# Kernel optimization log

Measured on AMD Instinct MI355X. Metric: run time of the kernel, lower is better.

## Reference

```python
import jax, jax.numpy as jnp
import numpy as np

L, B, D, H, K = 1024, 64, 256, 256, 4  # nodes, batch, input dim, hidden dim, heap arity


def _build_tree_schedule():
    # Deterministic 4-ary heap tree: parent(i) = (i-1)//K; children 4i+1..4i+4.
    # First K//2 children are 'left', last K//2 are 'right'. Pad slots use index L
    # (a sentinel zero row). Levels are processed deepest-first (leaves -> root).
    depth = np.zeros(L, dtype=np.int64)
    for i in range(1, L):
        depth[i] = depth[(i - 1) // K] + 1
    n_levels = int(depth.max()) + 1
    levels = [np.where(depth == d)[0] for d in range(n_levels)]
    M = max(len(lv) for lv in levels)
    level_nodes = np.full((n_levels, M), L, dtype=np.int32)
    child_idx = np.full((n_levels, M, K), L, dtype=np.int32)
    for d, lv in enumerate(levels):
        level_nodes[d, : len(lv)] = lv
        for j, n in enumerate(lv):
            for c in range(K):
                cc = K * n + c + 1
                if cc < L:
                    child_idx[d, j, c] = cc
    return jnp.asarray(level_nodes), jnp.asarray(child_idx)


def setup_inputs() -> dict:
    key = jax.random.key(0)
    ks = jax.random.split(key, 9)
    level_nodes, child_idx = _build_tree_schedule()
    sD = 1.0 / np.sqrt(D).astype(np.float32)
    sH = 1.0 / np.sqrt(H).astype(np.float32)
    return {
        "inputs": jax.random.normal(ks[0], (L, B, D), jnp.float32),
        "level_nodes": level_nodes,
        "child_idx": child_idx,
        "W_gih": jax.random.normal(ks[1], (5 * H, D), jnp.float32) * sD,
        "b_gih": jax.random.normal(ks[2], (5 * H,), jnp.float32) * sD,
        "W_glh": jax.random.normal(ks[3], (5 * H, H), jnp.float32) * sH,
        "W_grh": jax.random.normal(ks[4], (5 * H, H), jnp.float32) * sH,
        "W_cih": jax.random.normal(ks[5], (H, D), jnp.float32) * sD,
        "b_cih": jax.random.normal(ks[6], (H,), jnp.float32) * sD,
        "W_clh": jax.random.normal(ks[7], (H, H), jnp.float32) * sH,
        "W_crh": jax.random.normal(ks[8], (H, H), jnp.float32) * sH,
    }


def _tree_gru(inputs, level_nodes, child_idx, W_gih, b_gih, W_glh, W_grh,
              W_cih, b_cih, W_clh, W_crh):
    Ln, Bn, Dn = inputs.shape
    Hn = W_cih.shape[0]
    # Sentinel zero row at index Ln for padded node/child slots.
    inp_p = jnp.concatenate([inputs, jnp.zeros((1, Bn, Dn), inputs.dtype)], axis=0)
    h = jnp.zeros((Bn, Ln + 1, Hn), inputs.dtype)
    n_levels = level_nodes.shape[0]
    half = K // 2
    for d in range(n_levels - 1, -1, -1):  # leaves first, root last
        nodes = level_nodes[d]             # [M]
        ch = child_idx[d]                  # [M, K]
        # gather + sum child hidden states per side
        left_h = h[:, ch[:, 0]] + h[:, ch[:, 1]]      # [B, M, H]
        right_h = h[:, ch[:, half]] + h[:, ch[:, half + 1]]
        x = jnp.transpose(inp_p[nodes], (1, 0, 2))    # [B, M, D]
        gates = jax.nn.sigmoid(x @ W_gih.T + b_gih + left_h @ W_glh.T + right_h @ W_grh.T)
        rl, rr, zl, zr, z = jnp.split(gates, 5, axis=-1)
        cell = jnp.tanh(x @ W_cih.T + b_cih + (rl * left_h) @ W_clh.T + (rr * right_h) @ W_crh.T)
        hidden = zl * left_h + zr * right_h + z * cell
        h = h.at[:, nodes].set(hidden)
        h = h.at[:, Ln].set(0.0)  # keep sentinel row zero (padded writes land here)
    hn = h[:, :Ln]  # [B, L, H]
    # original output order: nodes 1..L-1 then root (node 0)
    outputs = jnp.concatenate([hn[:, 1:], hn[:, :1]], axis=1)
    return outputs, hn[:, 0]


def reference(inputs, level_nodes, child_idx, W_gih, b_gih, W_glh, W_grh,
              W_cih, b_cih, W_clh, W_crh):
    return _tree_gru(inputs, level_nodes, child_idx, W_gih, b_gih, W_glh, W_grh,
                     W_cih, b_cih, W_clh, W_crh)
```

## Files before the change

kernel.cpp:

```cpp
#include <hip/hip_runtime.h>


#define L_TOT 1024

typedef __attribute__((ext_vector_type(8))) short short8;
typedef __attribute__((ext_vector_type(4))) short short4v;
typedef __attribute__((ext_vector_type(4))) float f32x4;

static __device__ __forceinline__ float bf2f(unsigned short u) {
  unsigned int x = ((unsigned int)u) << 16;
  return __builtin_bit_cast(float, x);
}
static __device__ __forceinline__ unsigned short f2bf(float f) {
  unsigned int u = __builtin_bit_cast(unsigned int, f);
  u += 0x7fffu + ((u >> 16) & 1u);
  return (unsigned short)(u >> 16);
}
static __device__ __forceinline__ float sigmf(float x) { return 1.0f / (1.0f + __expf(-x)); }
static __device__ __forceinline__ float tanhf_(float x) { return 2.0f / (1.0f + __expf(-2.0f * x)) - 1.0f; }

static __device__ __forceinline__ void bar_lgkm() {
  asm volatile("s_waitcnt lgkmcnt(0)" ::: "memory");
  __builtin_amdgcn_s_barrier();
  __builtin_amdgcn_sched_barrier(0);
}

static __device__ __forceinline__ int swz_t(int orig, int nwg) {
  int q = nwg >> 3, r = nwg & 7, x = orig & 7, s = orig >> 3;
  return (x < r ? x * (q + 1) : r * (q + 1) + (x - r) * q) + s;
}

__global__ __launch_bounds__(256) void k_pre(
    const float* __restrict__ in,
    const float* __restrict__ Wgih, const float* __restrict__ Wglh, const float* __restrict__ Wgrh,
    const float* __restrict__ Wcih, const float* __restrict__ Wclh, const float* __restrict__ Wcrh,
    unsigned short* __restrict__ xb, unsigned short* __restrict__ Wg,
    unsigned short* __restrict__ Wc, unsigned short* __restrict__ Wl,
    unsigned short* __restrict__ hb) {
  int t = blockIdx.x * 256 + threadIdx.x;
  if (t < 524288) {
    const float* s = in + (size_t)t * 8;
    short8 v;
#pragma unroll
    for (int j = 0; j < 8; ++j) v[j] = (short)f2bf(s[j]);
    *(short8*)(xb + (size_t)t * 8) = v;
  }
  const int NG = 1280 * 768;
  const int NC = 256 * 768;
  const int NL = 512 * 256;
  if (t < NG) {
    int g = t / 768, k = t % 768;
    float v = (k < 256) ? Wgih[g * 256 + k] : ((k < 512) ? Wglh[g * 256 + k - 256] : Wgrh[g * 256 + k - 512]);
    Wg[t] = f2bf(v);
  } else if (t < NG + NC) {
    int t2 = t - NG;
    int g = t2 / 768, k = t2 % 768;
    float v = (k < 256) ? Wcih[g * 256 + k] : ((k < 512) ? Wclh[g * 256 + k - 256] : Wcrh[g * 256 + k - 512]);
    Wc[t2] = f2bf(v);
  } else if (t < NG + NC + NL) {
    int t2 = t - NG - NC;
    int n = t2 >> 8, k = t2 & 255;
    int g = n >> 4;
    int hc = (g >> 1) * 16 + (n & 15);
    float v = (g & 1) ? Wcih[hc * 256 + k] : Wgih[(1024 + hc) * 256 + k];
    Wl[t2] = f2bf(v);
  }
  if (t < 16384) hb[(size_t)1024 * 16384 + t] = 0;
}

__global__ __launch_bounds__(256) void k_prep(const unsigned short* __restrict__ hb,
                                              unsigned short* __restrict__ lh,
                                              unsigned short* __restrict__ rh,
                                              int rows, int row_off, int lvl_start) {
  int t = blockIdx.x * 256 + threadIdx.x;
  if (t >= rows * 32) return;
  int r = t >> 5, k8 = (t & 31) << 3;
  int gr = row_off + r;
  int node = lvl_start + (gr >> 6);
  int b = gr & 63;
  int cb = 4 * node + 1;
  int c0 = cb, c1 = cb + 1, c2 = cb + 2, c3 = cb + 3;
  c0 = (c0 < L_TOT) ? c0 : L_TOT;
  c1 = (c1 < L_TOT) ? c1 : L_TOT;
  c2 = (c2 < L_TOT) ? c2 : L_TOT;
  c3 = (c3 < L_TOT) ? c3 : L_TOT;
  const short8 v0 = *(const short8*)(hb + (size_t)c0 * 16384 + b * 256 + k8);
  const short8 v1 = *(const short8*)(hb + (size_t)c1 * 16384 + b * 256 + k8);
  const short8 v2 = *(const short8*)(hb + (size_t)c2 * 16384 + b * 256 + k8);
  const short8 v3 = *(const short8*)(hb + (size_t)c3 * 16384 + b * 256 + k8);
  short8 ol, orr;
#pragma unroll
  for (int j = 0; j < 8; ++j) {
    ol[j] = (short)f2bf(bf2f((unsigned short)v0[j]) + bf2f((unsigned short)v1[j]));
    orr[j] = (short)f2bf(bf2f((unsigned short)v2[j]) + bf2f((unsigned short)v3[j]));
  }
  *(short8*)(lh + (size_t)r * 256 + k8) = ol;
  *(short8*)(rh + (size_t)r * 256 + k8) = orr;
}

template <int EPI>
static __device__ __forceinline__ void gemm_body(
    const float* __restrict__ Af,
    const unsigned short* __restrict__ Aseg0,
    const unsigned short* __restrict__ Aseg1,
    const unsigned short* __restrict__ Aseg2,
    const unsigned short* __restrict__ Wt, const float* __restrict__ bias,
    const float* __restrict__ bias2,
    int rows, int row_off, int lvl_start, int NT, int nwg,
    const unsigned short* __restrict__ lh, const unsigned short* __restrict__ rh,
    unsigned short* __restrict__ a2l, unsigned short* __restrict__ a2r,
    unsigned short* __restrict__ p1, unsigned short* __restrict__ p2,
    unsigned short* __restrict__ zb, unsigned short* __restrict__ hb,
    float* __restrict__ out) {
  constexpr int NKT = (EPI == 2) ? 4 : 12;
  constexpr int WSTRIDE = (EPI == 2) ? 256 : 768;
  constexpr int LR = 72;
  int t = swz_t(blockIdx.x, nwg);
  int tm = t / NT, tn = t % NT;
  const int tid = threadIdx.x, lane = tid & 63, wave = tid >> 6;
  const int wr = wave >> 1, wcl = wave & 1;

  __shared__ unsigned short As[2][128 * LR];
  __shared__ unsigned short Bs[2][128 * LR];

  f32x4 acc[2][4];
#pragma unroll
  for (int i = 0; i < 2; ++i)
#pragma unroll
    for (int j = 0; j < 4; ++j) {
      f32x4 zv = {0.f, 0.f, 0.f, 0.f};
      acc[i][j] = zv;
    }

  const unsigned short* segs[3] = {Aseg0, Aseg1, Aseg2};
  const int srow = tid >> 3;
  const int scol = (tid & 7) * 8;

  short8 rva[3][2], rvb[3][2];
  f32x4 fva[3][2][2];

  auto LOADK = [&](int kt, int s) {
    int ko = (kt & 3) * 64;
#pragma unroll
    for (int i = 0; i < 2; ++i) {
      int row = srow + i * 64;
      if (EPI == 2) {
        const float* ap = Af + (size_t)(tm * 128 + row) * 256 + ko + scol;
        fva[s][i][0] = *(const f32x4*)(ap);
        fva[s][i][1] = *(const f32x4*)(ap + 4);
      } else {
        const unsigned short* segp = segs[kt >> 2];
        rva[s][i] = *(const short8*)(segp + (size_t)(tm * 128 + row) * 256 + ko + scol);
      }
      rvb[s][i] = *(const short8*)(Wt + (size_t)(tn * 128 + row) * WSTRIDE + kt * 64 + scol);
    }
  };
  auto WRITEK = [&](int s, int buf) {
#pragma unroll
    for (int i = 0; i < 2; ++i) {
      int row = srow + i * 64;
      short8 v;
      if (EPI == 2) {
#pragma unroll
        for (int j = 0; j < 4; ++j) {
          v[j] = (short)f2bf(fva[s][i][0][j]);
          v[j + 4] = (short)f2bf(fva[s][i][1][j]);
        }
      } else {
        v = rva[s][i];
      }
      *(short8*)(&As[buf][row * LR + scol]) = v;
      *(short8*)(&Bs[buf][row * LR + scol]) = rvb[s][i];
    }
  };

  LOADK(0, 0);
  LOADK(1, 1);
  if (NKT > 2) LOADK(2, 2);
  WRITEK(0, 0);
  bar_lgkm();

#pragma unroll
  for (int kt = 0; kt < NKT; ++kt) {
    const int cur = kt & 1;
    if (kt + 1 < NKT) WRITEK((kt + 1) % 3, cur ^ 1);
    if (kt + 3 < NKT) LOADK(kt + 3, kt % 3);
#pragma unroll
    for (int kk = 0; kk < 2; ++kk) {
      short8 af[2], bf[4];
#pragma unroll
      for (int mf = 0; mf < 2; ++mf)
        af[mf] = *(const short8*)(&As[cur][(wr * 32 + mf * 16 + (lane & 15)) * LR + kk * 32 + (lane >> 4) * 8]);
#pragma unroll
      for (int nf = 0; nf < 4; ++nf)
        bf[nf] = *(const short8*)(&Bs[cur][(wcl * 64 + nf * 16 + (lane & 15)) * LR + kk * 32 + (lane >> 4) * 8]);
#pragma unroll
      for (int mf = 0; mf < 2; ++mf)
#pragma unroll
        for (int nf = 0; nf < 4; ++nf)
          acc[mf][nf] = __builtin_amdgcn_mfma_f32_16x16x32_bf16(bf[nf], af[mf], acc[mf][nf], 0, 0, 0);
    }
    if (kt + 1 < NKT) bar_lgkm();
  }

  if (EPI == 2) {
#pragma unroll
    for (int nfp = 0; nfp < 2; ++nfp) {
      int nz = nfp * 2;
      int g = tn * 8 + wcl * 4 + nz;
      int hcq = (g >> 1) * 16 + (lane >> 4) * 4;
      f32x4 bzv = *(const f32x4*)(bias + 1024 + hcq);
      f32x4 bcv = *(const f32x4*)(bias2 + hcq);
#pragma unroll
      for (int mf = 0; mf < 2; ++mf) {
        int r = tm * 128 + wr * 32 + mf * 16 + (lane & 15);
        int node = 256 + (r >> 6), b = r & 63;
        short4v hv;
        float4 ov;
#pragma unroll
        for (int j = 0; j < 4; ++j) {
          float h = sigmf(acc[mf][nz][j] + bzv[j]) * tanhf_(acc[mf][nz + 1][j] + bcv[j]);
          hv[j] = (short)f2bf(h);
          ((float*)&ov)[j] = h;
        }
        *(short4v*)(hb + (size_t)node * 16384 + b * 256 + hcq) = hv;
        *(float4*)(out + (size_t)b * 262144 + (size_t)(node - 1) * 256 + hcq) = ov;
      }
    }
    return;
  }
#pragma unroll
  for (int nf = 0; nf < 4; ++nf) {
    int colq = tn * 128 + wcl * 64 + nf * 16 + (lane >> 4) * 4;
    f32x4 bsv = *(const f32x4*)(bias + colq);
    if (EPI == 0) {
      int ck = colq >> 8;
      int gcq = colq & 255;
#pragma unroll
      for (int mf = 0; mf < 2; ++mf) {
        int r = tm * 128 + wr * 32 + mf * 16 + (lane & 15);
        if (r < rows) {
          size_t idx = (size_t)r * 256 + gcq;
          f32x4 s;
#pragma unroll
          for (int j = 0; j < 4; ++j) s[j] = sigmf(acc[mf][nf][j] + bsv[j]);
          short4v res;
          if (ck == 4) {
#pragma unroll
            for (int j = 0; j < 4; ++j) res[j] = (short)f2bf(s[j]);
            *(short4v*)(zb + idx) = res;
          } else {
            const unsigned short* src = (ck == 0 || ck == 2) ? lh : rh;
            short4v hv = *(const short4v*)(src + idx);
#pragma unroll
            for (int j = 0; j < 4; ++j) res[j] = (short)f2bf(s[j] * bf2f((unsigned short)hv[j]));
            if (ck == 0)      *(short4v*)(a2l + idx) = res;
            else if (ck == 1) *(short4v*)(a2r + idx) = res;
            else if (ck == 2) *(short4v*)(p1 + idx) = res;
            else              *(short4v*)(p2 + idx) = res;
          }
        }
      }
    } else {
#pragma unroll
      for (int mf = 0; mf < 2; ++mf) {
        int r = tm * 128 + wr * 32 + mf * 16 + (lane & 15);
        if (r < rows) {
          size_t idx = (size_t)r * 256 + colq;
          short4v p1v = *(const short4v*)(p1 + idx);
          short4v p2v = *(const short4v*)(p2 + idx);
          short4v zbv = *(const short4v*)(zb + idx);
          int gr = row_off + r;
          int node = lvl_start + (gr >> 6);
          int b = gr & 63;
          short4v hv;
          float4 ov;
#pragma unroll
          for (int j = 0; j < 4; ++j) {
            float cell = tanhf_(acc[mf][nf][j] + bsv[j]);
            float hid = bf2f((unsigned short)p1v[j]) + bf2f((unsigned short)p2v[j]) +
                        bf2f((unsigned short)zbv[j]) * cell;
            hv[j] = (short)f2bf(hid);
            ((float*)&ov)[j] = hid;
          }
          *(short4v*)(hb + (size_t)node * 16384 + b * 256 + colq) = hv;
          int jj = node ? (node - 1) : 1023;
          *(float4*)(out + (size_t)b * 262144 + (size_t)jj * 256 + colq) = ov;
          if (node == 0)
            *(float4*)(out + 16777216 + (size_t)b * 256 + colq) = ov;
        }
      }
    }
  }
}

__global__ __launch_bounds__(512, 4) void k_gates(
    const unsigned short* __restrict__ A0, const unsigned short* __restrict__ A1,
    const unsigned short* __restrict__ A2, const unsigned short* __restrict__ Wt,
    const float* __restrict__ bias, int rows, int row_off, int lvl_start, int nwg,
    const unsigned short* __restrict__ lh, const unsigned short* __restrict__ rh,
    unsigned short* __restrict__ a2l, unsigned short* __restrict__ a2r,
    unsigned short* __restrict__ p1, unsigned short* __restrict__ p2,
    unsigned short* __restrict__ zb) {
  gemm_body<0>(nullptr, A0, A1, A2, Wt, bias, nullptr, rows, row_off, lvl_start, 10, nwg,
               lh, rh, a2l, a2r, p1, p2, zb, nullptr, nullptr);
}

__global__ __launch_bounds__(512, 4) void k_cell(
    const unsigned short* __restrict__ A0, const unsigned short* __restrict__ A1,
    const unsigned short* __restrict__ A2, const unsigned short* __restrict__ Wt,
    const float* __restrict__ bias, int rows, int row_off, int lvl_start, int nwg,
    const unsigned short* __restrict__ p1, const unsigned short* __restrict__ p2,
    const unsigned short* __restrict__ zb, unsigned short* __restrict__ hb,
    float* __restrict__ out) {
  gemm_body<1>(nullptr, A0, A1, A2, Wt, bias, nullptr, rows, row_off, lvl_start, 2, nwg,
               nullptr, nullptr, nullptr, nullptr, (unsigned short*)p1,
               (unsigned short*)p2, (unsigned short*)zb, hb, out);
}

__global__ __launch_bounds__(512, 4) void k_leaf(
    const float* __restrict__ X, const unsigned short* __restrict__ Wl,
    const float* __restrict__ bg, const float* __restrict__ bc, int nwg,
    unsigned short* __restrict__ hb, float* __restrict__ out) {
  gemm_body<2>(X, nullptr, nullptr, nullptr, Wl, bg, bc, 49152, 0, 0, 4, nwg,
               nullptr, nullptr, nullptr, nullptr, nullptr, nullptr, nullptr, hb, out);
}

extern "C" void kernel_launch(void* const* d_in, const int* in_sizes, int n_in,
                              void* d_out, int out_size, void* d_ws, size_t ws_size,
                              hipStream_t stream) {
  const float* inputs = (const float*)d_in[0];
  const float* W_gih = (const float*)d_in[3];
  const float* b_gih = (const float*)d_in[4];
  const float* W_glh = (const float*)d_in[5];
  const float* W_grh = (const float*)d_in[6];
  const float* W_cih = (const float*)d_in[7];
  const float* b_cih = (const float*)d_in[8];
  const float* W_clh = (const float*)d_in[9];
  const float* W_crh = (const float*)d_in[10];
  float* out = (float*)d_out;

  char* ws = (char*)d_ws;
  size_t cur = 0;
  auto alloc = [&](size_t bytes) -> char* {
    char* p = ws + cur;
    cur += (bytes + 255) & ~(size_t)255;
    return p;
  };

  unsigned short* xb = (unsigned short*)alloc((size_t)(16384 + 128) * 256 * 2);
  unsigned short* hb = (unsigned short*)alloc((size_t)1025 * 16384 * 2);
  unsigned short* Wg = (unsigned short*)alloc((size_t)1280 * 768 * 2);
  unsigned short* Wc = (unsigned short*)alloc((size_t)256 * 768 * 2);
  unsigned short* Wl = (unsigned short*)alloc((size_t)512 * 256 * 2);

  size_t rem = (ws_size > cur) ? (ws_size - cur) : 0;
  long long rcap = (long long)(rem / (7 * 512 + 64));
  rcap = (rcap / 128) * 128;
  int Rchunk = (int)((rcap < 11008) ? rcap : 11008);
  if (Rchunk < 128) Rchunk = 128;

  unsigned short* lh  = (unsigned short*)alloc((size_t)Rchunk * 512);
  unsigned short* rh  = (unsigned short*)alloc((size_t)Rchunk * 512);
  unsigned short* a2l = (unsigned short*)alloc((size_t)Rchunk * 512);
  unsigned short* a2r = (unsigned short*)alloc((size_t)Rchunk * 512);
  unsigned short* p1  = (unsigned short*)alloc((size_t)Rchunk * 512);
  unsigned short* p2  = (unsigned short*)alloc((size_t)Rchunk * 512);
  unsigned short* zb  = (unsigned short*)alloc((size_t)Rchunk * 512);

  k_pre<<<5120, 256, 0, stream>>>(inputs, W_gih, W_glh, W_grh, W_cih, W_clh, W_crh,
                                  xb, Wg, Wc, Wl, hb);

  k_leaf<<<1536, 512, 0, stream>>>(inputs + (size_t)16384 * 256, Wl, b_gih, b_cih, 1536, hb, out);

  static const int LSi[5] = {0, 1, 5, 21, 85};
  static const int LCi[5] = {1, 4, 16, 64, 171};

  for (int d = 4; d >= 0; --d) {
    int rows_lvl = LCi[d] * 64;
    for (int off = 0; off < rows_lvl; off += Rchunk) {
      int rows = rows_lvl - off;
      if (rows > Rchunk) rows = Rchunk;
      int tmn = (rows + 127) / 128;
      int pgrid = (rows * 32 + 255) / 256;
      k_prep<<<pgrid, 256, 0, stream>>>(hb, lh, rh, rows, off, LSi[d]);
      const unsigned short* xseg = xb + (size_t)(LSi[d] * 64 + off) * 256;
      int nwg_g = tmn * 10;
      k_gates<<<nwg_g, 512, 0, stream>>>(xseg, lh, rh, Wg, b_gih, rows, off, LSi[d], nwg_g,
                                         lh, rh, a2l, a2r, p1, p2, zb);
      int nwg_c = tmn * 2;
      k_cell<<<nwg_c, 512, 0, stream>>>(xseg, a2l, a2r, Wc, b_cih, rows, off, LSi[d], nwg_c,
                                        p1, p2, zb, hb, out);
    }
  }
}
```

Measured before the change: 255.7 us.

## Rewrite leaf kernel to keep A rows in registers and sweep all N tiles

The leaf GEMM becomes a dedicated kernel. Each workgroup loads and converts its 128-row fp32 input block to bf16 once, keeps it in registers, and loops over all four N tiles, streaming only weight tiles through double-buffered LDS. This removes the fourfold re-read and re-conversion of the fp32 leaf inputs and cuts the grid from 1536 to 384 workgroups. The cost is lower parallelism and higher register pressure, since each wave holds 8 A fragments plus 8 accumulators.

```diff
diff --git a/kernel.cpp b/kernel.cpp
--- a/kernel.cpp
+++ b/kernel.cpp
@@ -100,20 +100,17 @@
 
 template <int EPI>
 static __device__ __forceinline__ void gemm_body(
-    const float* __restrict__ Af,
     const unsigned short* __restrict__ Aseg0,
     const unsigned short* __restrict__ Aseg1,
     const unsigned short* __restrict__ Aseg2,
     const unsigned short* __restrict__ Wt, const float* __restrict__ bias,
-    const float* __restrict__ bias2,
     int rows, int row_off, int lvl_start, int NT, int nwg,
     const unsigned short* __restrict__ lh, const unsigned short* __restrict__ rh,
     unsigned short* __restrict__ a2l, unsigned short* __restrict__ a2r,
     unsigned short* __restrict__ p1, unsigned short* __restrict__ p2,
     unsigned short* __restrict__ zb, unsigned short* __restrict__ hb,
     float* __restrict__ out) {
-  constexpr int NKT = (EPI == 2) ? 4 : 12;
-  constexpr int WSTRIDE = (EPI == 2) ? 256 : 768;
+  constexpr int NKT = 12;
   constexpr int LR = 72;
   int t = swz_t(blockIdx.x, nwg);
   int tm = t / NT, tn = t % NT;
@@ -137,46 +134,29 @@
   const int scol = (tid & 7) * 8;
 
   short8 rva[3][2], rvb[3][2];
-  f32x4 fva[3][2][2];
 
   auto LOADK = [&](int kt, int s) {
     int ko = (kt & 3) * 64;
+    const unsigned short* segp = segs[kt >> 2];
 #pragma unroll
     for (int i = 0; i < 2; ++i) {
       int row = srow + i * 64;
-      if (EPI == 2) {
-        const float* ap = Af + (size_t)(tm * 128 + row) * 256 + ko + scol;
-        fva[s][i][0] = *(const f32x4*)(ap);
-        fva[s][i][1] = *(const f32x4*)(ap + 4);
-      } else {
-        const unsigned short* segp = segs[kt >> 2];
-        rva[s][i] = *(const short8*)(segp + (size_t)(tm * 128 + row) * 256 + ko + scol);
-      }
-      rvb[s][i] = *(const short8*)(Wt + (size_t)(tn * 128 + row) * WSTRIDE + kt * 64 + scol);
+      rva[s][i] = *(const short8*)(segp + (size_t)(tm * 128 + row) * 256 + ko + scol);
+      rvb[s][i] = *(const short8*)(Wt + (size_t)(tn * 128 + row) * 768 + kt * 64 + scol);
     }
   };
   auto WRITEK = [&](int s, int buf) {
 #pragma unroll
     for (int i = 0; i < 2; ++i) {
       int row = srow + i * 64;
-      short8 v;
-      if (EPI == 2) {
-#pragma unroll
-        for (int j = 0; j < 4; ++j) {
-          v[j] = (short)f2bf(fva[s][i][0][j]);
-          v[j + 4] = (short)f2bf(fva[s][i][1][j]);
-        }
-      } else {
-        v = rva[s][i];
-      }
-      *(short8*)(&As[buf][row * LR + scol]) = v;
+      *(short8*)(&As[buf][row * LR + scol]) = rva[s][i];
       *(short8*)(&Bs[buf][row * LR + scol]) = rvb[s][i];
     }
   };
 
   LOADK(0, 0);
   LOADK(1, 1);
-  if (NKT > 2) LOADK(2, 2);
+  LOADK(2, 2);
   WRITEK(0, 0);
   bar_lgkm();
 
@@ -203,32 +183,6 @@
     if (kt + 1 < NKT) bar_lgkm();
   }
 
-  if (EPI == 2) {
-#pragma unroll
-    for (int nfp = 0; nfp < 2; ++nfp) {
-      int nz = nfp * 2;
-      int g = tn * 8 + wcl * 4 + nz;
-      int hcq = (g >> 1) * 16 + (lane >> 4) * 4;
-      f32x4 bzv = *(const f32x4*)(bias + 1024 + hcq);
-      f32x4 bcv = *(const f32x4*)(bias2 + hcq);
-#pragma unroll
-      for (int mf = 0; mf < 2; ++mf) {
-        int r = tm * 128 + wr * 32 + mf * 16 + (lane & 15);
-        int node = 256 + (r >> 6), b = r & 63;
-        short4v hv;
-        float4 ov;
-#pragma unroll
-        for (int j = 0; j < 4; ++j) {
-          float h = sigmf(acc[mf][nz][j] + bzv[j]) * tanhf_(acc[mf][nz + 1][j] + bcv[j]);
-          hv[j] = (short)f2bf(h);
-          ((float*)&ov)[j] = h;
-        }
-        *(short4v*)(hb + (size_t)node * 16384 + b * 256 + hcq) = hv;
-        *(float4*)(out + (size_t)b * 262144 + (size_t)(node - 1) * 256 + hcq) = ov;
-      }
-    }
-    return;
-  }
 #pragma unroll
   for (int nf = 0; nf < 4; ++nf) {
     int colq = tn * 128 + wcl * 64 + nf * 16 + (lane >> 4) * 4;
@@ -302,7 +256,7 @@
     unsigned short* __restrict__ a2l, unsigned short* __restrict__ a2r,
     unsigned short* __restrict__ p1, unsigned short* __restrict__ p2,
     unsigned short* __restrict__ zb) {
-  gemm_body<0>(nullptr, A0, A1, A2, Wt, bias, nullptr, rows, row_off, lvl_start, 10, nwg,
+  gemm_body<0>(A0, A1, A2, Wt, bias, rows, row_off, lvl_start, 10, nwg,
                lh, rh, a2l, a2r, p1, p2, zb, nullptr, nullptr);
 }
 
@@ -313,17 +267,108 @@
     const unsigned short* __restrict__ p1, const unsigned short* __restrict__ p2,
     const unsigned short* __restrict__ zb, unsigned short* __restrict__ hb,
     float* __restrict__ out) {
-  gemm_body<1>(nullptr, A0, A1, A2, Wt, bias, nullptr, rows, row_off, lvl_start, 2, nwg,
+  gemm_body<1>(A0, A1, A2, Wt, bias, rows, row_off, lvl_start, 2, nwg,
                nullptr, nullptr, nullptr, nullptr, (unsigned short*)p1,
                (unsigned short*)p2, (unsigned short*)zb, hb, out);
 }
 
 __global__ __launch_bounds__(512, 4) void k_leaf(
-    const float* __restrict__ X, const unsigned short* __restrict__ Wl,
+    const float* __restrict__ Af, const unsigned short* __restrict__ Wl,
     const float* __restrict__ bg, const float* __restrict__ bc, int nwg,
     unsigned short* __restrict__ hb, float* __restrict__ out) {
-  gemm_body<2>(X, nullptr, nullptr, nullptr, Wl, bg, bc, 49152, 0, 0, 4, nwg,
-               nullptr, nullptr, nullptr, nullptr, nullptr, nullptr, nullptr, hb, out);
+  constexpr int LR = 72;
+  int tm = swz_t(blockIdx.x, nwg);
+  const int tid = threadIdx.x, lane = tid & 63, wave = tid >> 6;
+
+  __shared__ unsigned short Bs[2][128 * LR];
+
+  const int arow = tm * 128 + wave * 16 + (lane & 15);
+  short8 afr[8];
+  {
+    const float* ap = Af + (size_t)arow * 256 + (lane >> 4) * 8;
+#pragma unroll
+    for (int kk = 0; kk < 8; ++kk) {
+      f32x4 f0 = *(const f32x4*)(ap + kk * 32);
+      f32x4 f1 = *(const f32x4*)(ap + kk * 32 + 4);
+      short8 v;
+#pragma unroll
+      for (int j = 0; j < 4; ++j) {
+        v[j] = (short)f2bf(f0[j]);
+        v[j + 4] = (short)f2bf(f1[j]);
+      }
+      afr[kk] = v;
+    }
+  }
+
+  const int srow = tid >> 3;
+  const int scol = (tid & 7) * 8;
+  short8 rvb[2][2];
+
+  auto LOADB = [&](int s, int set) {
+    int tn = s >> 2, kt = s & 3;
+#pragma unroll
+    for (int i = 0; i < 2; ++i)
+      rvb[set][i] = *(const short8*)(Wl + (size_t)(tn * 128 + srow + i * 64) * 256 + kt * 64 + scol);
+  };
+  auto WRITEB = [&](int set, int buf) {
+#pragma unroll
+    for (int i = 0; i < 2; ++i)
+      *(short8*)(&Bs[buf][(srow + i * 64) * LR + scol]) = rvb[set][i];
+  };
+
+  LOADB(0, 0);
+  LOADB(1, 1);
+  WRITEB(0, 0);
+  bar_lgkm();
+
+  f32x4 acc[8];
+
+#pragma unroll
+  for (int s = 0; s < 16; ++s) {
+    const int cur = s & 1;
+    const int kt = s & 3;
+    if (kt == 0) {
+#pragma unroll
+      for (int nf = 0; nf < 8; ++nf) {
+        f32x4 zv = {0.f, 0.f, 0.f, 0.f};
+        acc[nf] = zv;
+      }
+    }
+    if (s + 1 < 16) WRITEB((s + 1) & 1, cur ^ 1);
+    if (s + 2 < 16) LOADB(s + 2, s & 1);
+#pragma unroll
+    for (int kk2 = 0; kk2 < 2; ++kk2) {
+      int kk = kt * 2 + kk2;
+      short8 bf[8];
+#pragma unroll
+      for (int nf = 0; nf < 8; ++nf)
+        bf[nf] = *(const short8*)(&Bs[cur][(nf * 16 + (lane & 15)) * LR + kk2 * 32 + (lane >> 4) * 8]);
+#pragma unroll
+      for (int nf = 0; nf < 8; ++nf)
+        acc[nf] = __builtin_amdgcn_mfma_f32_16x16x32_bf16(bf[nf], afr[kk], acc[nf], 0, 0, 0);
+    }
+    if (s + 1 < 16) bar_lgkm();
+    if (kt == 3) {
+      int tn = s >> 2;
+      int node = 256 + (arow >> 6), b = arow & 63;
+#pragma unroll
+      for (int nfp = 0; nfp < 4; ++nfp) {
+        int hcq = (tn * 4 + nfp) * 16 + (lane >> 4) * 4;
+        f32x4 bzv = *(const f32x4*)(bg + 1024 + hcq);
+        f32x4 bcv = *(const f32x4*)(bc + hcq);
+        short4v hv;
+        float4 ov;
+#pragma unroll
+        for (int j = 0; j < 4; ++j) {
+          float h = sigmf(acc[2 * nfp][j] + bzv[j]) * tanhf_(acc[2 * nfp + 1][j] + bcv[j]);
+          hv[j] = (short)f2bf(h);
+          ((float*)&ov)[j] = h;
+        }
+        *(short4v*)(hb + (size_t)node * 16384 + b * 256 + hcq) = hv;
+        *(float4*)(out + (size_t)b * 262144 + (size_t)(node - 1) * 256 + hcq) = ov;
+      }
+    }
+  }
 }
 
 extern "C" void kernel_launch(void* const* d_in, const int* in_sizes, int n_in,
@@ -371,7 +416,7 @@
   k_pre<<<5120, 256, 0, stream>>>(inputs, W_gih, W_glh, W_grh, W_cih, W_clh, W_crh,
                                   xb, Wg, Wc, Wl, hb);
 
-  k_leaf<<<1536, 512, 0, stream>>>(inputs + (size_t)16384 * 256, Wl, b_gih, b_cih, 1536, hb, out);
+  k_leaf<<<384, 512, 0, stream>>>(inputs + (size_t)16384 * 256, Wl, b_gih, b_cih, 384, hb, out);
 
   static const int LSi[5] = {0, 1, 5, 21, 85};
   static const int LCi[5] = {1, 4, 16, 64, 171};
```

After: 265.5 us. +3.8%, slower.

## Add register-prefetched double-buffered GEMM body for small-grid internal levels

Applied to the files above, without the earlier changes.

Adds a new 128x128 GEMM body that prefetches K tiles into registers two steps ahead and double-buffers them through LDS, so global-load latency overlaps MFMA work. The gates kernel uses it when the grid is small (at most 256 workgroups), and the cell kernel always uses it. The aim is to cut latency-bound time on the small upper-level GEMMs where there are too few workgroups to hide memory stalls. In exchange it uses much more LDS and more registers, so occupancy drops to 2 blocks per CU.

```diff
diff --git a/kernel.cpp b/kernel.cpp
--- a/kernel.cpp
+++ b/kernel.cpp
@@ -294,6 +294,157 @@
   }
 }
 
+template <int EPI>
+static __device__ __forceinline__ void gemm_body128(
+    const unsigned short* __restrict__ Aseg0,
+    const unsigned short* __restrict__ Aseg1,
+    const unsigned short* __restrict__ Aseg2,
+    const unsigned short* __restrict__ Wt, const float* __restrict__ bias,
+    int rows, int row_off, int lvl_start, int NT, int nwg,
+    const unsigned short* __restrict__ lh, const unsigned short* __restrict__ rh,
+    unsigned short* __restrict__ a2l, unsigned short* __restrict__ a2r,
+    unsigned short* __restrict__ p1, unsigned short* __restrict__ p2,
+    unsigned short* __restrict__ zb, unsigned short* __restrict__ hb,
+    float* __restrict__ out) {
+  constexpr int NKT = 6;
+  constexpr int LR = 136;
+  int t = swz_t(blockIdx.x, nwg);
+  int tm = t / NT, tn = t % NT;
+  const int tid = threadIdx.x, lane = tid & 63, wave = tid >> 6;
+  const int wr = wave >> 1, wcl = wave & 1;
+
+  __shared__ unsigned short As[2][128 * LR];
+  __shared__ unsigned short Bs[2][128 * LR];
+
+  f32x4 acc[2][4];
+#pragma unroll
+  for (int i = 0; i < 2; ++i)
+#pragma unroll
+    for (int j = 0; j < 4; ++j) {
+      f32x4 zv = {0.f, 0.f, 0.f, 0.f};
+      acc[i][j] = zv;
+    }
+
+  const unsigned short* segs[3] = {Aseg0, Aseg1, Aseg2};
+
+  short8 rva[2][4], rvb[2][4];
+
+  auto LOADK = [&](int kt, int s) {
+    const unsigned short* segp = segs[kt >> 1];
+    int ko = (kt & 1) * 128;
+#pragma unroll
+    for (int i = 0; i < 4; ++i) {
+      int ch = tid + 512 * i;
+      int row = ch >> 4;
+      int col = (ch & 15) * 8;
+      rva[s][i] = *(const short8*)(segp + (size_t)(tm * 128 + row) * 256 + ko + col);
+      rvb[s][i] = *(const short8*)(Wt + (size_t)(tn * 128 + row) * 768 + kt * 128 + col);
+    }
+  };
+  auto WRITEK = [&](int s, int buf) {
+#pragma unroll
+    for (int i = 0; i < 4; ++i) {
+      int ch = tid + 512 * i;
+      int row = ch >> 4;
+      int col = (ch & 15) * 8;
+      *(short8*)(&As[buf][row * LR + col]) = rva[s][i];
+      *(short8*)(&Bs[buf][row * LR + col]) = rvb[s][i];
+    }
+  };
+
+  LOADK(0, 0);
+  LOADK(1, 1);
+  WRITEK(0, 0);
+  bar_lgkm();
+
+#pragma unroll
+  for (int kt = 0; kt < NKT; ++kt) {
+    const int cur = kt & 1;
+    if (kt + 1 < NKT) WRITEK((kt + 1) & 1, cur ^ 1);
+    if (kt + 2 < NKT) LOADK(kt + 2, kt & 1);
+#pragma unroll
+    for (int kk = 0; kk < 4; ++kk) {
+      short8 af[2], bf[4];
+#pragma unroll
+      for (int mf = 0; mf < 2; ++mf)
+        af[mf] = *(const short8*)(&As[cur][(wr * 32 + mf * 16 + (lane & 15)) * LR + kk * 32 + (lane >> 4) * 8]);
+#pragma unroll
+      for (int nf = 0; nf < 4; ++nf)
+        bf[nf] = *(const short8*)(&Bs[cur][(wcl * 64 + nf * 16 + (lane & 15)) * LR + kk * 32 + (lane >> 4) * 8]);
+#pragma unroll
+      for (int mf = 0; mf < 2; ++mf)
+#pragma unroll
+        for (int nf = 0; nf < 4; ++nf)
+          acc[mf][nf] = __builtin_amdgcn_mfma_f32_16x16x32_bf16(bf[nf], af[mf], acc[mf][nf], 0, 0, 0);
+    }
+    if (kt + 1 < NKT) bar_lgkm();
+  }
+
+#pragma unroll
+  for (int nf = 0; nf < 4; ++nf) {
+    int colq = tn * 128 + wcl * 64 + nf * 16 + (lane >> 4) * 4;
+    f32x4 bsv = *(const f32x4*)(bias + colq);
+    if (EPI == 0) {
+      int ck = colq >> 8;
+      int gcq = colq & 255;
+#pragma unroll
+      for (int mf = 0; mf < 2; ++mf) {
+        int r = tm * 128 + wr * 32 + mf * 16 + (lane & 15);
+        if (r < rows) {
+          size_t idx = (size_t)r * 256 + gcq;
+          f32x4 s;
+#pragma unroll
+          for (int j = 0; j < 4; ++j) s[j] = sigmf(acc[mf][nf][j] + bsv[j]);
+          short4v res;
+          if (ck == 4) {
+#pragma unroll
+            for (int j = 0; j < 4; ++j) res[j] = (short)f2bf(s[j]);
+            *(short4v*)(zb + idx) = res;
+          } else {
+            const unsigned short* src = (ck == 0 || ck == 2) ? lh : rh;
+            short4v hv = *(const short4v*)(src + idx);
+#pragma unroll
+            for (int j = 0; j < 4; ++j) res[j] = (short)f2bf(s[j] * bf2f((unsigned short)hv[j]));
+            if (ck == 0)      *(short4v*)(a2l + idx) = res;
+            else if (ck == 1) *(short4v*)(a2r + idx) = res;
+            else if (ck == 2) *(short4v*)(p1 + idx) = res;
+            else              *(short4v*)(p2 + idx) = res;
+          }
+        }
+      }
+    } else {
+#pragma unroll
+      for (int mf = 0; mf < 2; ++mf) {
+        int r = tm * 128 + wr * 32 + mf * 16 + (lane & 15);
+        if (r < rows) {
+          size_t idx = (size_t)r * 256 + colq;
+          short4v p1v = *(const short4v*)(p1 + idx);
+          short4v p2v = *(const short4v*)(p2 + idx);
+          short4v zbv = *(const short4v*)(zb + idx);
+          int gr = row_off + r;
+          int node = lvl_start + (gr >> 6);
+          int b = gr & 63;
+          short4v hv;
+          float4 ov;
+#pragma unroll
+          for (int j = 0; j < 4; ++j) {
+            float cell = tanhf_(acc[mf][nf][j] + bsv[j]);
+            float hid = bf2f((unsigned short)p1v[j]) + bf2f((unsigned short)p2v[j]) +
+                        bf2f((unsigned short)zbv[j]) * cell;
+            hv[j] = (short)f2bf(hid);
+            ((float*)&ov)[j] = hid;
+          }
+          *(short4v*)(hb + (size_t)node * 16384 + b * 256 + colq) = hv;
+          int jj = node ? (node - 1) : 1023;
+          *(float4*)(out + (size_t)b * 262144 + (size_t)jj * 256 + colq) = ov;
+          if (node == 0)
+            *(float4*)(out + 16777216 + (size_t)b * 256 + colq) = ov;
+        }
+      }
+    }
+  }
+}
+
 __global__ __launch_bounds__(512, 4) void k_gates(
     const unsigned short* __restrict__ A0, const unsigned short* __restrict__ A1,
     const unsigned short* __restrict__ A2, const unsigned short* __restrict__ Wt,
@@ -306,16 +457,28 @@
                lh, rh, a2l, a2r, p1, p2, zb, nullptr, nullptr);
 }
 
-__global__ __launch_bounds__(512, 4) void k_cell(
+__global__ __launch_bounds__(512, 2) void k_gates_s(
+    const unsigned short* __restrict__ A0, const unsigned short* __restrict__ A1,
+    const unsigned short* __restrict__ A2, const unsigned short* __restrict__ Wt,
+    const float* __restrict__ bias, int rows, int row_off, int lvl_start, int nwg,
+    const unsigned short* __restrict__ lh, const unsigned short* __restrict__ rh,
+    unsigned short* __restrict__ a2l, unsigned short* __restrict__ a2r,
+    unsigned short* __restrict__ p1, unsigned short* __restrict__ p2,
+    unsigned short* __restrict__ zb) {
+  gemm_body128<0>(A0, A1, A2, Wt, bias, rows, row_off, lvl_start, 10, nwg,
+                  lh, rh, a2l, a2r, p1, p2, zb, nullptr, nullptr);
+}
+
+__global__ __launch_bounds__(512, 2) void k_cell_s(
     const unsigned short* __restrict__ A0, const unsigned short* __restrict__ A1,
     const unsigned short* __restrict__ A2, const unsigned short* __restrict__ Wt,
     const float* __restrict__ bias, int rows, int row_off, int lvl_start, int nwg,
     const unsigned short* __restrict__ p1, const unsigned short* __restrict__ p2,
     const unsigned short* __restrict__ zb, unsigned short* __restrict__ hb,
     float* __restrict__ out) {
-  gemm_body<1>(nullptr, A0, A1, A2, Wt, bias, nullptr, rows, row_off, lvl_start, 2, nwg,
-               nullptr, nullptr, nullptr, nullptr, (unsigned short*)p1,
-               (unsigned short*)p2, (unsigned short*)zb, hb, out);
+  gemm_body128<1>(A0, A1, A2, Wt, bias, rows, row_off, lvl_start, 2, nwg,
+                  nullptr, nullptr, nullptr, nullptr, (unsigned short*)p1,
+                  (unsigned short*)p2, (unsigned short*)zb, hb, out);
 }
 
 __global__ __launch_bounds__(512, 4) void k_leaf(
@@ -386,11 +549,15 @@
       k_prep<<<pgrid, 256, 0, stream>>>(hb, lh, rh, rows, off, LSi[d]);
       const unsigned short* xseg = xb + (size_t)(LSi[d] * 64 + off) * 256;
       int nwg_g = tmn * 10;
-      k_gates<<<nwg_g, 512, 0, stream>>>(xseg, lh, rh, Wg, b_gih, rows, off, LSi[d], nwg_g,
-                                         lh, rh, a2l, a2r, p1, p2, zb);
+      if (nwg_g <= 256)
+        k_gates_s<<<nwg_g, 512, 0, stream>>>(xseg, lh, rh, Wg, b_gih, rows, off, LSi[d], nwg_g,
+                                             lh, rh, a2l, a2r, p1, p2, zb);
+      else
+        k_gates<<<nwg_g, 512, 0, stream>>>(xseg, lh, rh, Wg, b_gih, rows, off, LSi[d], nwg_g,
+                                           lh, rh, a2l, a2r, p1, p2, zb);
       int nwg_c = tmn * 2;
-      k_cell<<<nwg_c, 512, 0, stream>>>(xseg, a2l, a2r, Wc, b_cih, rows, off, LSi[d], nwg_c,
-                                        p1, p2, zb, hb, out);
-    }
-  }
-}
+      k_cell_s<<<nwg_c, 512, 0, stream>>>(xseg, a2l, a2r, Wc, b_cih, rows, off, LSi[d], nwg_c,
+                                          p1, p2, zb, hb, out);
+    }
+  }
+}
```

Result: no change. 254.9 us (median of 2 runs) (-0.3%).
